# Performance work log

Hardware: AMD Instinct MI355X
Metric: run time of the kernel (lower is better)

The kernel has to match this reference:

```python
import jax, jax.numpy as jnp
import numpy as np

C = 256
HEADS = 4
HIDDEN = 4 * C  # LeFF default hidden_dim = dim*4
EPS = 1e-5


def conv2d(x, w, pad):
    # x: [B,C,H,W], w: [O,I,kh,kw]
    return jax.lax.conv_general_dilated(
        x, w, window_strides=(1, 1), padding=[(pad, pad), (pad, pad)],
        dimension_numbers=('NCHW', 'OIHW', 'NCHW'))


def dwconv2d(x, w, pad):
    # depthwise: w: [C,1,kh,kw], groups = C
    return jax.lax.conv_general_dilated(
        x, w, window_strides=(1, 1), padding=[(pad, pad), (pad, pad)],
        dimension_numbers=('NCHW', 'OIHW', 'NCHW'),
        feature_group_count=x.shape[1])


def conv1x1(x, w):
    # w: [O, I]; pointwise conv as einsum
    return jnp.einsum('oi,bihw->bohw', w, x)


def layernorm(x, weight, bias):
    # WithBias LayerNorm over channel dim of NCHW (matches to_3d -> LN over c)
    mu = jnp.mean(x, axis=1, keepdims=True)
    var = jnp.mean((x - mu) ** 2, axis=1, keepdims=True)
    xn = (x - mu) / jnp.sqrt(var + EPS)
    return xn * weight[None, :, None, None] + bias[None, :, None, None]


def mhsa(q, k, v, heads):
    # q,k,v: [B,C,H,W] -> global attention over N = H*W tokens
    b, c, h, w = q.shape
    d = c // heads
    scale = d ** -0.5
    def split(t):
        return t.reshape(b, heads, d, h * w)  # [B,H,d,N]
    qh, kh, vh = split(q), split(k), split(v)
    attn = jnp.einsum('bhdn,bhdm->bhnm', qh, kh) * scale  # [B,H,N,N]
    attn = jax.nn.softmax(attn, axis=-1)
    out = jnp.einsum('bhnm,bhdm->bhdn', attn, vh)
    return out.reshape(b, c, h, w)


def self_attn(x, w_qkv, w_proj, heads):
    qkv = conv1x1(x, w_qkv)  # [B,3C,H,W]
    q, k, v = jnp.split(qkv, 3, axis=1)
    return conv1x1(mhsa(q, k, v, heads), w_proj)


def cross_attn(qf, kvf, w_q, w_k, w_v, w_proj, heads):
    q = conv1x1(qf, w_q)
    k = conv1x1(kvf, w_k)
    v = conv1x1(kvf, w_v)
    return conv1x1(mhsa(q, k, v, heads), w_proj)


def leff(x, w_in, w_dw, w_out):
    h = conv1x1(x, w_in)
    h = dwconv2d(h, w_dw, pad=1)
    h = jax.nn.gelu(h, approximate=False)  # torch nn.GELU() = exact erf
    return conv1x1(h, w_out)


def setup_inputs() -> dict:
    key = jax.random.key(0)
    ks = jax.random.split(key, 32)
    s = 0.02
    inp = {
        'aop_feat': jax.random.normal(ks[0], (8, C, 32, 32), jnp.float32),
        'dop_feat': jax.random.normal(ks[1], (8, C, 32, 32), jnp.float32),
        'w_qconv': jax.random.normal(ks[2], (C, C, 3, 3), jnp.float32) * s,
        'w_kvconv': jax.random.normal(ks[3], (C, C, 5, 5), jnp.float32) * s,
        'lnq1_w': jnp.ones((C,), jnp.float32), 'lnq1_b': jnp.zeros((C,), jnp.float32),
        'lnkv1_w': jnp.ones((C,), jnp.float32), 'lnkv1_b': jnp.zeros((C,), jnp.float32),
        'lnq2_w': jnp.ones((C,), jnp.float32), 'lnq2_b': jnp.zeros((C,), jnp.float32),
        'lnkv2_w': jnp.ones((C,), jnp.float32), 'lnkv2_b': jnp.zeros((C,), jnp.float32),
        'lnffn_w': jnp.ones((C,), jnp.float32), 'lnffn_b': jnp.zeros((C,), jnp.float32),
        'saq_qkv': jax.random.normal(ks[4], (3 * C, C), jnp.float32) * s,
        'saq_proj': jax.random.normal(ks[5], (C, C), jnp.float32) * s,
        'sakv_qkv': jax.random.normal(ks[6], (3 * C, C), jnp.float32) * s,
        'sakv_proj': jax.random.normal(ks[7], (C, C), jnp.float32) * s,
        'ca_q': jax.random.normal(ks[8], (C, C), jnp.float32) * s,
        'ca_k': jax.random.normal(ks[9], (C, C), jnp.float32) * s,
        'ca_v': jax.random.normal(ks[10], (C, C), jnp.float32) * s,
        'ca_proj': jax.random.normal(ks[11], (C, C), jnp.float32) * s,
        'leff_in': jax.random.normal(ks[12], (HIDDEN, C), jnp.float32) * s,
        'leff_dw': jax.random.normal(ks[13], (HIDDEN, 1, 3, 3), jnp.float32) * s,
        'leff_out': jax.random.normal(ks[14], (C, HIDDEN), jnp.float32) * s,
    }
    return inp


def reference(aop_feat, dop_feat, w_qconv, w_kvconv,
              lnq1_w, lnq1_b, lnkv1_w, lnkv1_b, lnq2_w, lnq2_b,
              lnkv2_w, lnkv2_b, lnffn_w, lnffn_b,
              saq_qkv, saq_proj, sakv_qkv, sakv_proj,
              ca_q, ca_k, ca_v, ca_proj,
              leff_in, leff_dw, leff_out):
    # q branch
    q_branch = conv2d(aop_feat, w_qconv, pad=1)
    q_branch = q_branch + self_attn(layernorm(q_branch, lnq1_w, lnq1_b), saq_qkv, saq_proj, HEADS)
    q = layernorm(q_branch, lnq2_w, lnq2_b)
    # kv branch
    kv_branch = conv2d(dop_feat, w_kvconv, pad=2)
    kv_branch = kv_branch + self_attn(layernorm(kv_branch, lnkv1_w, lnkv1_b), sakv_qkv, sakv_proj, HEADS)
    kv = layernorm(kv_branch, lnkv2_w, lnkv2_b)
    # cross attention + FFN
    x = q_branch + cross_attn(q, kv, ca_q, ca_k, ca_v, ca_proj, HEADS)
    x = x + leff(layernorm(x, lnffn_w, lnffn_b), leff_in, leff_dw, leff_out)
    return x
```

## Files before the change

### kernel.cpp

```cpp
#include <hip/hip_runtime.h>
#include <hip/hip_bf16.h>


using bf16 = __hip_bfloat16;
typedef short v8s __attribute__((ext_vector_type(8)));
typedef float v4f  __attribute__((ext_vector_type(4)));

static __device__ __forceinline__ float bf2f(bf16 x) { return __bfloat162float(x); }
static __device__ __forceinline__ float us2f(unsigned short u)
{ union { unsigned int i; float f; } x; x.i = ((unsigned)u) << 16; return x.f; }
static __device__ __forceinline__ unsigned short f2us(float f)
{ bf16 h = __float2bfloat16(f); return *(unsigned short*)&h; }
static __device__ __forceinline__ float ldi(const void* p, size_t i, int isbf)
{ return isbf ? bf2f(((const bf16*)p)[i]) : ((const float*)p)[i]; }

__global__ void detect_kernel(const unsigned short* p, int* flag)
{
    if (threadIdx.x == 0 && blockIdx.x == 0)
        *flag = (p[0] == 0x3F80) ? 1 : 0;
}

struct CvtArgs { const void* src[20]; unsigned off[21]; };

__global__ __launch_bounds__(256) void cvt_lin(CvtArgs a, const int* __restrict__ flag,
                                               bf16* __restrict__ dst)
{
    unsigned e = blockIdx.x * 256u + threadIdx.x;
    int isbf = *flag;
    int s = 0;
    while (e >= a.off[s + 1]) ++s;
    dst[e] = __float2bfloat16(ldi(a.src[s], e - a.off[s], isbf));
}

__global__ __launch_bounds__(256) void tcvt2(const void* __restrict__ s0,
                                             const void* __restrict__ s1,
                                             const int* __restrict__ flag,
                                             bf16* __restrict__ d0,
                                             bf16* __restrict__ d1)
{
    __shared__ float T[64][65];
    const void* src = (blockIdx.z < 8) ? s0 : s1;
    bf16* dst       = (blockIdx.z < 8) ? d0 : d1;
    int hw0 = blockIdx.x * 64, c0 = blockIdx.y * 64, b = blockIdx.z & 7;
    int t = threadIdx.x, isbf = *flag;
    int c = t >> 2, x16 = (t & 3) * 16;
    size_t sbase = ((size_t)b * 256 + c0 + c) * 1024 + hw0 + x16;
#pragma unroll
    for (int j = 0; j < 16; ++j) T[c][x16 + j] = ldi(src, sbase + j, isbf);
    __syncthreads();
    int hw = t >> 2, c16 = (t & 3) * 16;
    bf16* dp = dst + ((size_t)(b << 10) + hw0 + hw) * 256 + c0 + c16;
#pragma unroll
    for (int j = 0; j < 16; ++j) dp[j] = __float2bfloat16(T[c16 + j][hw]);
}

__global__ __launch_bounds__(256) void repack_all(
    const void* __restrict__ W3, const void* __restrict__ W5,
    const void* __restrict__ Wdw, const int* __restrict__ flag,
    bf16* __restrict__ R3, bf16* __restrict__ R5, bf16* __restrict__ Rdw)
{
    int idx = blockIdx.x * 256 + threadIdx.x;
    int isbf = *flag;
    if (idx < 589824) {
        int ci = idx & 255, o = (idx >> 8) & 255, khkw = idx >> 16;
        int kh = khkw / 3, kw = khkw % 3;
        R3[idx] = __float2bfloat16(
            ldi(W3, (((size_t)o * 256 + ci) * 3 + kh) * 3 + kw, isbf));
    } else if (idx < 2228224) {
        int j = idx - 589824;
        int ci = j & 255, o = (j >> 8) & 255, khkw = j >> 16;
        int kh = khkw / 5, kw = khkw % 5;
        R5[j] = __float2bfloat16(
            ldi(W5, (((size_t)o * 256 + ci) * 5 + kh) * 5 + kw, isbf));
    } else {
        int j = idx - 2228224;
        int c = j & 1023, tap = j >> 10;
        Rdw[j] = __float2bfloat16(ldi(Wdw, (size_t)c * 9 + tap, isbf));
    }
}

static __device__ __forceinline__ void mgemm_core(
    const short* __restrict__ MA, const short* __restrict__ MB,
    bf16* __restrict__ Yb, float* __restrict__ Yf, bf16* __restrict__ Y2,
    const bf16* __restrict__ R, int K, int mode, int Ochan,
    short As[64][72], short Bs[64][72])
{
    int m0 = blockIdx.x * 64, n0 = blockIdx.y * 64;
    int t = threadIdx.x, lane = t & 63, wv = t >> 6;
    int l15 = lane & 15, quad = lane >> 4;
    int srow = t >> 2, scol = (t & 3) * 16;

    const short* pa = &MA[(size_t)(m0 + srow) * K + scol];
    const short* pb = &MB[(size_t)(n0 + srow) * K + scol];

    v4f acc[4] = {};
    v8s ra0 = *(const v8s*)&pa[0], ra1 = *(const v8s*)&pa[8];
    v8s rb0 = *(const v8s*)&pb[0], rb1 = *(const v8s*)&pb[8];

    for (int k0 = 0; k0 < K; k0 += 64) {
        if (k0) __syncthreads();
        *(v8s*)&As[srow][scol]     = ra0;
        *(v8s*)&As[srow][scol + 8] = ra1;
        *(v8s*)&Bs[srow][scol]     = rb0;
        *(v8s*)&Bs[srow][scol + 8] = rb1;
        __syncthreads();
        if (k0 + 64 < K) {
            ra0 = *(const v8s*)&pa[k0 + 64];
            ra1 = *(const v8s*)&pa[k0 + 72];
            rb0 = *(const v8s*)&pb[k0 + 64];
            rb1 = *(const v8s*)&pb[k0 + 72];
        }
#pragma unroll
        for (int kk = 0; kk < 2; ++kk) {
            v8s a = *(const v8s*)&As[wv * 16 + l15][kk * 32 + quad * 8];
#pragma unroll
            for (int nt = 0; nt < 4; ++nt) {
                v8s b = *(const v8s*)&Bs[nt * 16 + l15][kk * 32 + quad * 8];
                acc[nt] = __builtin_amdgcn_mfma_f32_16x16x32_bf16(a, b, acc[nt], 0, 0, 0);
            }
        }
    }

#pragma unroll
    for (int nt = 0; nt < 4; ++nt)
#pragma unroll
        for (int r = 0; r < 4; ++r) {
            int mm = m0 + wv * 16 + quad * 4 + r;
            int nn = n0 + nt * 16 + l15;
            float v = acc[nt][r];
            if (mode == 0) {
                size_t off = (size_t)mm * Ochan + nn;
                if (R) v += bf2f(R[off]);
                Yb[off] = __float2bfloat16(v);
            } else if (mode == 1) {
                Yb[((size_t)(nn >> 10) * Ochan + mm) * 1024 + (nn & 1023)] =
                    __float2bfloat16(v);
            } else if (mode == 2) {
                Yf[((size_t)(nn >> 10) * Ochan + mm) * 1024 + (nn & 1023)] =
                    v + bf2f(R[(size_t)nn * 256 + mm]);
            } else if (mode == 3) {
                if (mm < 512) Yb[(size_t)nn * 512 + mm] = __float2bfloat16(v);
                else Y2[((size_t)(nn >> 10) * 256 + (mm - 512)) * 1024 + (nn & 1023)] =
                         __float2bfloat16(v);
            } else {
                Yb[(size_t)nn * 512 + Ochan + mm] = __float2bfloat16(v);
            }
        }
}

__global__ __launch_bounds__(256) void mgemm(
    const short* __restrict__ MA, const short* __restrict__ MB,
    bf16* __restrict__ Yb, float* __restrict__ Yf, bf16* __restrict__ Y2,
    const bf16* __restrict__ R, int K, int mode, int Ochan)
{
    __shared__ short As[64][72], Bs[64][72];
    mgemm_core(MA, MB, Yb, Yf, Y2, R, K, mode, Ochan, As, Bs);
}

struct GA { const short* A; const short* B; bf16* Yb; float* Yf; bf16* Y2;
            const bf16* R; int K; int mode; int Oc; };
struct GA3 { GA g[3]; };

__global__ __launch_bounds__(256) void mgemm_z(GA3 P)
{
    __shared__ short As[64][72], Bs[64][72];
    const GA& a = P.g[blockIdx.z];
    mgemm_core(a.A, a.B, a.Yb, a.Yf, a.Y2, a.R, a.K, a.mode, a.Oc, As, Bs);
}

template <int KS, int PAD>
static __device__ __forceinline__ void mconv128_core(
    const short* __restrict__ Xn, const short* __restrict__ Wr,
    bf16* __restrict__ Y, float* __restrict__ Yf,
    short As[128][72], short Bs[128][72],
    int p0, int o0, int kbeg, int kend)
{
    int t = threadIdx.x, lane = t & 63, wv = t >> 6;
    int l15 = lane & 15, quad = lane >> 4;
    int wm = wv >> 1, wn = wv & 1;
    int srow = t >> 1, scol = (t & 1) * 32;

    int p  = p0 + srow;
    int hw = p & 1023, hh = hw >> 5, ww = hw & 31;
    size_t ib = ((size_t)(p >> 10)) << 10;

    v4f acc[4][4] = {};
    v8s ra[4], rb[4];

    auto ldk = [&](int k0) {
        int khkw = k0 >> 8;
        int kh = khkw / KS, kw = khkw % KS;
        int hi = hh + kh - PAD, wi = ww + kw - PAD;
        int aci = (k0 & 255) + scol;
        v8s z = {0, 0, 0, 0, 0, 0, 0, 0};
        ra[0] = z; ra[1] = z; ra[2] = z; ra[3] = z;
        if ((unsigned)hi < 32u && (unsigned)wi < 32u) {
            const short* sa = &Xn[(ib + (hi << 5) + wi) * 256 + aci];
            ra[0] = *(const v8s*)&sa[0];  ra[1] = *(const v8s*)&sa[8];
            ra[2] = *(const v8s*)&sa[16]; ra[3] = *(const v8s*)&sa[24];
        }
        const short* sb = &Wr[((size_t)khkw * 256 + o0 + srow) * 256 + (k0 & 255) + scol];
        rb[0] = *(const v8s*)&sb[0];  rb[1] = *(const v8s*)&sb[8];
        rb[2] = *(const v8s*)&sb[16]; rb[3] = *(const v8s*)&sb[24];
    };

    ldk(kbeg);

    for (int k0 = kbeg; k0 < kend; k0 += 64) {
        if (k0 != kbeg) __syncthreads();
        *(v8s*)&As[srow][scol]      = ra[0];
        *(v8s*)&As[srow][scol + 8]  = ra[1];
        *(v8s*)&As[srow][scol + 16] = ra[2];
        *(v8s*)&As[srow][scol + 24] = ra[3];
        *(v8s*)&Bs[srow][scol]      = rb[0];
        *(v8s*)&Bs[srow][scol + 8]  = rb[1];
        *(v8s*)&Bs[srow][scol + 16] = rb[2];
        *(v8s*)&Bs[srow][scol + 24] = rb[3];
        __syncthreads();
        if (k0 + 64 < kend) ldk(k0 + 64);
#pragma unroll
        for (int kk = 0; kk < 2; ++kk) {
            v8s af[4], bf[4];
#pragma unroll
            for (int i = 0; i < 4; ++i)
                af[i] = *(const v8s*)&As[wm * 64 + i * 16 + l15][kk * 32 + quad * 8];
#pragma unroll
            for (int i = 0; i < 4; ++i)
                bf[i] = *(const v8s*)&Bs[wn * 64 + i * 16 + l15][kk * 32 + quad * 8];
#pragma unroll
            for (int mt = 0; mt < 4; ++mt)
#pragma unroll
                for (int nt = 0; nt < 4; ++nt)
                    acc[mt][nt] = __builtin_amdgcn_mfma_f32_16x16x32_bf16(
                        af[mt], bf[nt], acc[mt][nt], 0, 0, 0);
        }
    }

#pragma unroll
    for (int mt = 0; mt < 4; ++mt)
#pragma unroll
        for (int nt = 0; nt < 4; ++nt)
#pragma unroll
            for (int r = 0; r < 4; ++r) {
                int pp = p0 + wm * 64 + mt * 16 + quad * 4 + r;
                int oo = o0 + wn * 64 + nt * 16 + l15;
                if (Yf) Yf[(size_t)pp * 256 + oo] = acc[mt][nt][r];
                else    Y[(size_t)pp * 256 + oo] = __float2bfloat16(acc[mt][nt][r]);
            }
}

__global__ __launch_bounds__(256) void mconv2(
    const short* __restrict__ Xa, const short* __restrict__ Wa, bf16* __restrict__ Ya,
    const short* __restrict__ Xb, const short* __restrict__ Wb,
    float* __restrict__ P0, float* __restrict__ P1, float* __restrict__ P2)
{
    __shared__ short As[128][72];
    __shared__ short Bs[128][72];
    int wg = blockIdx.x;
    if (wg < 128) {
        mconv128_core<3, 1>(Xa, Wa, Ya, nullptr, As, Bs,
                            (wg & 63) * 128, (wg >> 6) * 128, 0, 2304);
    } else {
        int j = wg - 128;
        int part = j >> 7, xy = j & 127;
        float* Pf = (part == 0) ? P0 : (part == 1) ? P1 : P2;
        int kbeg = part * 2112;
        int kend = (part < 2) ? kbeg + 2112 : 6400;
        mconv128_core<5, 2>(Xb, Wb, nullptr, Pf, As, Bs,
                            (xy & 63) * 128, (xy >> 6) * 128, kbeg, kend);
    }
}

__global__ __launch_bounds__(256) void addcvt3(
    const float* __restrict__ A, const float* __restrict__ B,
    const float* __restrict__ C, bf16* __restrict__ Y)
{
    int i = (blockIdx.x * 256 + threadIdx.x) * 4;
    float4 a = *(const float4*)&A[i];
    float4 b = *(const float4*)&B[i];
    float4 c = *(const float4*)&C[i];
    ushort4 o;
    o.x = f2us(a.x + b.x + c.x);
    o.y = f2us(a.y + b.y + c.y);
    o.z = f2us(a.z + b.z + c.z);
    o.w = f2us(a.w + b.w + c.w);
    *(ushort4*)((unsigned short*)Y + i) = o;
}

static __device__ __forceinline__ void attn_core(
    const bf16* __restrict__ QK, const bf16* __restrict__ V,
    bf16* __restrict__ Out, int b, int h, int n0,
    short Ps[4][16][72], short Ks[64][72], short Vs[64][72])
{
    int t = threadIdx.x, lane = t & 63, wv = t >> 6;
    int l15 = lane & 15, quad = lane >> 4;
    int srow = t >> 2, scol = (t & 3) * 16;

    const short* qk = (const short*)QK;
    const short* vp = (const short*)V + ((size_t)b * 256 + h * 64) * 1024;

    size_t qrow = ((size_t)b * 1024 + n0 + wv * 16 + l15) * 512 + h * 64;
    v8s qf0 = *(const v8s*)&qk[qrow + quad * 8];
    v8s qf1 = *(const v8s*)&qk[qrow + 32 + quad * 8];

    v4f oacc[4] = {};
    float mi[4], li[4], nmiSC[4];
#pragma unroll
    for (int r = 0; r < 4; ++r) { mi[r] = -1e30f; li[r] = 0.f; nmiSC[r] = 0.f; }
    const float SC = 0.18033688011112042f;

    const short* kbase = &qk[((size_t)b * 1024 + srow) * 512 + 256 + h * 64 + scol];
    const short* vbase = vp + (size_t)srow * 1024 + scol;

    v8s rk0 = *(const v8s*)&kbase[0], rk1 = *(const v8s*)&kbase[8];
    v8s rv0 = *(const v8s*)&vbase[0], rv1 = *(const v8s*)&vbase[8];

    for (int m0 = 0; m0 < 1024; m0 += 64) {
        if (m0) __syncthreads();
        *(v8s*)&Ks[srow][scol]     = rk0;
        *(v8s*)&Ks[srow][scol + 8] = rk1;
        *(v8s*)&Vs[srow][scol]     = rv0;
        *(v8s*)&Vs[srow][scol + 8] = rv1;
        __syncthreads();
        if (m0 + 64 < 1024) {
            rk0 = *(const v8s*)&kbase[(size_t)(m0 + 64) * 512];
            rk1 = *(const v8s*)&kbase[(size_t)(m0 + 64) * 512 + 8];
            rv0 = *(const v8s*)&vbase[m0 + 64];
            rv1 = *(const v8s*)&vbase[m0 + 72];
        }

        v4f sacc[4];
        __builtin_amdgcn_s_setprio(1);
#pragma unroll
        for (int ct = 0; ct < 4; ++ct) {
            v8s kf0 = *(const v8s*)&Ks[ct * 16 + l15][quad * 8];
            v8s kf1 = *(const v8s*)&Ks[ct * 16 + l15][32 + quad * 8];
            v4f z = {0.f, 0.f, 0.f, 0.f};
            z = __builtin_amdgcn_mfma_f32_16x16x32_bf16(qf0, kf0, z, 0, 0, 0);
            z = __builtin_amdgcn_mfma_f32_16x16x32_bf16(qf1, kf1, z, 0, 0, 0);
            sacc[ct] = z;
        }
        __builtin_amdgcn_s_setprio(0);

        float pr[4];
#pragma unroll
        for (int r = 0; r < 4; ++r)
            pr[r] = fmaxf(fmaxf(sacc[0][r], sacc[1][r]),
                          fmaxf(sacc[2][r], sacc[3][r]));
        bool grow = (pr[0] > mi[0]) | (pr[1] > mi[1]) |
                    (pr[2] > mi[2]) | (pr[3] > mi[3]);
        if (__any(grow)) {
#pragma unroll
            for (int mk = 1; mk <= 8; mk <<= 1)
#pragma unroll
                for (int r = 0; r < 4; ++r)
                    pr[r] = fmaxf(pr[r], __shfl_xor(pr[r], mk));
#pragma unroll
            for (int r = 0; r < 4; ++r) {
                float mn = fmaxf(mi[r], pr[r]);
                float al = exp2f((mi[r] - mn) * SC);
                mi[r] = mn;
                nmiSC[r] = -mn * SC;
                li[r] *= al;
#pragma unroll
                for (int dt = 0; dt < 4; ++dt) oacc[dt][r] *= al;
            }
        }

#pragma unroll
        for (int ct = 0; ct < 4; ++ct)
#pragma unroll
            for (int r = 0; r < 4; ++r) {
                float pvv = exp2f(fmaf(sacc[ct][r], SC, nmiSC[r]));
                li[r] += pvv;
                Ps[wv][quad * 4 + r][ct * 16 + l15] = (short)f2us(pvv);
            }

        v8s pf0 = *(const v8s*)&Ps[wv][l15][quad * 8];
        v8s pf1 = *(const v8s*)&Ps[wv][l15][32 + quad * 8];
        __builtin_amdgcn_s_setprio(1);
#pragma unroll
        for (int dt = 0; dt < 4; ++dt) {
            v8s vf0 = *(const v8s*)&Vs[dt * 16 + l15][quad * 8];
            v8s vf1 = *(const v8s*)&Vs[dt * 16 + l15][32 + quad * 8];
            oacc[dt] = __builtin_amdgcn_mfma_f32_16x16x32_bf16(pf0, vf0, oacc[dt], 0, 0, 0);
            oacc[dt] = __builtin_amdgcn_mfma_f32_16x16x32_bf16(pf1, vf1, oacc[dt], 0, 0, 0);
        }
        __builtin_amdgcn_s_setprio(0);
    }

#pragma unroll
    for (int mk = 1; mk <= 8; mk <<= 1)
#pragma unroll
        for (int r = 0; r < 4; ++r)
            li[r] += __shfl_xor(li[r], mk);

    float linv[4];
#pragma unroll
    for (int r = 0; r < 4; ++r) linv[r] = 1.0f / li[r];
    size_t pb = (size_t)b * 1024 + n0 + wv * 16;
#pragma unroll
    for (int dt = 0; dt < 4; ++dt)
#pragma unroll
        for (int r = 0; r < 4; ++r)
            Out[(pb + quad * 4 + r) * 256 + h * 64 + dt * 16 + l15] =
                __float2bfloat16(oacc[dt][r] * linv[r]);
}

template <int NG>
__global__ __launch_bounds__(256) void attn_swz(
    const bf16* __restrict__ QK0, const bf16* __restrict__ V0, bf16* __restrict__ O0,
    const bf16* __restrict__ QK1, const bf16* __restrict__ V1, bf16* __restrict__ O1)
{
    __shared__ short Ps[4][16][72];
    __shared__ short Ks[64][72], Vs[64][72];
    int i = blockIdx.x;
    int xcd = i & 7, idx = i >> 3;
    int g = xcd * (NG / 8) + (idx >> 4);
    int n0 = (idx & 15) * 64;
    int h = g & 3, zz = g >> 2;
    int b = zz & 7;
    if (zz < 8) attn_core(QK0, V0, O0, b, h, n0, Ps, Ks, Vs);
    else        attn_core(QK1, V1, O1, b, h, n0, Ps, Ks, Vs);
}

static __device__ __forceinline__ void ln_row(
    const bf16* __restrict__ X, const bf16* __restrict__ g,
    const bf16* __restrict__ be, bf16* __restrict__ Y, size_t p)
{
    int lane = threadIdx.x & 63;
    const ushort4 u = *(const ushort4*)(X + p * 256 + lane * 4);
    float v0 = us2f(u.x), v1 = us2f(u.y), v2 = us2f(u.z), v3 = us2f(u.w);
    float s = v0 + v1 + v2 + v3;
    float ss = v0 * v0 + v1 * v1 + v2 * v2 + v3 * v3;
#pragma unroll
    for (int off = 32; off; off >>= 1) {
        s  += __shfl_xor(s, off);
        ss += __shfl_xor(ss, off);
    }
    float mu   = s * (1.0f / 256.0f);
    float var  = ss * (1.0f / 256.0f) - mu * mu;
    float rstd = rsqrtf(fmaxf(var, 0.0f) + 1e-5f);
    const ushort4 gu = *(const ushort4*)((const unsigned short*)g + lane * 4);
    const ushort4 bu = *(const ushort4*)((const unsigned short*)be + lane * 4);
    ushort4 o;
    o.x = f2us((v0 - mu) * rstd * us2f(gu.x) + us2f(bu.x));
    o.y = f2us((v1 - mu) * rstd * us2f(gu.y) + us2f(bu.y));
    o.z = f2us((v2 - mu) * rstd * us2f(gu.z) + us2f(bu.z));
    o.w = f2us((v3 - mu) * rstd * us2f(gu.w) + us2f(bu.w));
    *(ushort4*)(Y + p * 256 + lane * 4) = o;
}

__global__ __launch_bounds__(256) void ln_nhwc(
    const bf16* __restrict__ X, const bf16* __restrict__ g,
    const bf16* __restrict__ be, bf16* __restrict__ Y)
{
    int wv = threadIdx.x >> 6;
    ln_row(X, g, be, Y, (size_t)blockIdx.x * 4 + wv);
}

__global__ __launch_bounds__(256) void ln_nhwc2(
    const bf16* __restrict__ X0, const bf16* __restrict__ g0,
    const bf16* __restrict__ b0, bf16* __restrict__ Y0,
    const bf16* __restrict__ X1, const bf16* __restrict__ g1,
    const bf16* __restrict__ b1, bf16* __restrict__ Y1)
{
    int wv = threadIdx.x >> 6;
    int sel = blockIdx.x >> 11;
    size_t p = (size_t)(blockIdx.x & 2047) * 4 + wv;
    if (sel == 0) ln_row(X0, g0, b0, Y0, p);
    else          ln_row(X1, g1, b1, Y1, p);
}

__global__ __launch_bounds__(256) void dwgelu_nhwc(
    const bf16* __restrict__ H, const bf16* __restrict__ Wr,
    bf16* __restrict__ Y)
{
    int idx = blockIdx.x * 256 + threadIdx.x;
    int p = idx >> 7, c8 = (idx & 127) * 8;
    int hw = p & 1023, hh = hw >> 5, ww = hw & 31;
    size_t ib = ((size_t)(p >> 10)) << 10;
    float acc[8] = {};
#pragma unroll
    for (int kh = 0; kh < 3; ++kh)
#pragma unroll
        for (int kw = 0; kw < 3; ++kw) {
            int hi = hh + kh - 1, wi = ww + kw - 1;
            if ((unsigned)hi < 32u && (unsigned)wi < 32u) {
                v8s hv = *(const v8s*)((const short*)H + (ib + (hi << 5) + wi) * 1024 + c8);
                v8s wvv = *(const v8s*)((const short*)Wr + (kh * 3 + kw) * 1024 + c8);
#pragma unroll
                for (int j = 0; j < 8; ++j)
                    acc[j] = fmaf(us2f((unsigned short)wvv[j]),
                                  us2f((unsigned short)hv[j]), acc[j]);
            }
        }
    short ov[8];
#pragma unroll
    for (int j = 0; j < 8; ++j) {
        float x = acc[j];
        ov[j] = (short)f2us(0.5f * x * (1.0f + erff(x * 0.70710678118654752f)));
    }
    v8s o = {ov[0], ov[1], ov[2], ov[3], ov[4], ov[5], ov[6], ov[7]};
    *(v8s*)((short*)Y + (size_t)p * 1024 + c8) = o;
}

extern "C" void kernel_launch(void* const* d_in, const int* in_sizes, int n_in,
                              void* d_out, int out_size, void* d_ws, size_t ws_size,
                              hipStream_t stream)
{
    static const int  lidx[20] = {4,5,6,7,8,9,10,11,12,13,14,15,16,17,18,19,20,21,22,24};
    static const unsigned lsz[20] = {256,256,256,256,256,256,256,256,256,256,
                                     196608,65536,196608,65536,
                                     65536,65536,65536,65536,262144,262144};
    CvtArgs args;
    unsigned pre[21]; pre[0] = 0;
    for (int i = 0; i < 20; ++i) {
        args.src[i] = d_in[lidx[i]];
        pre[i + 1] = pre[i] + lsz[i];
    }
    for (int i = 0; i < 21; ++i) args.off[i] = pre[i];
    const unsigned ltot = pre[20];

    int*  flag  = (int*)d_ws;
    bf16* canon = (bf16*)d_ws + 128;
    bf16* cn[25];
    for (int i = 0; i < 20; ++i) cn[lidx[i]] = canon + pre[i];

    bf16* Wr3  = canon + ltot;
    bf16* Wr5  = Wr3 + 589824;
    bf16* Wdwr = Wr5 + 1638400;
    const size_t SZ = 2097152;
    bf16* slab = Wdwr + 9216;
    bf16* qb   = slab + 0 * SZ;
    bf16* kvb  = slab + 1 * SZ;
    bf16* t0   = slab + 2 * SZ;
    bf16* q    = slab + 3 * SZ;
    bf16* kv   = slab + 4 * SZ;
    bf16* QKb  = slab + 5 * SZ;
    bf16* Vb   = slab + 7 * SZ;
    bf16* t1   = slab + 8 * SZ;
    bf16* QK2  = slab + 9 * SZ;
    bf16* V2   = slab + 11 * SZ;
    bf16* aopT = slab + 9 * SZ;
    bf16* dopT = slab + 10 * SZ;
    bf16* hb   = slab + 3 * SZ;
    bf16* h2   = slab + 7 * SZ;
    float* P0f = (float*)(slab + 2 * SZ);
    float* P1f = (float*)(slab + 4 * SZ);
    float* P2f = (float*)(slab + 6 * SZ);
    float* out = (float*)d_out;

    dim3 blk(256);
    auto S = [](const bf16* p) { return (const short*)p; };

    detect_kernel<<<1, 64, 0, stream>>>((const unsigned short*)d_in[4], flag);
    cvt_lin<<<ltot / 256, blk, 0, stream>>>(args, flag, canon);
    tcvt2<<<dim3(16, 4, 16), blk, 0, stream>>>(d_in[0], d_in[1], flag, aopT, dopT);
    repack_all<<<8740, blk, 0, stream>>>(d_in[2], d_in[3], d_in[23], flag, Wr3, Wr5, Wdwr);

    mconv2<<<512, blk, 0, stream>>>(S(aopT), (const short*)Wr3, qb,
                                    S(dopT), (const short*)Wr5, P0f, P1f, P2f);
    addcvt3<<<2048, blk, 0, stream>>>(P0f, P1f, P2f, kvb);

    ln_nhwc2<<<4096, blk, 0, stream>>>(qb, cn[4], cn[5], t0,
                                       kvb, cn[6], cn[7], t1);
    GA3 P;
    P.g[0] = GA{S(cn[14]), S(t0), QKb, nullptr, Vb, nullptr, 256, 3, 0};
    P.g[1] = GA{S(cn[16]), S(t1), QK2, nullptr, V2, nullptr, 256, 3, 0};
    P.g[2] = P.g[1];
    mgemm_z<<<dim3(12, 128, 2), blk, 0, stream>>>(P);

    attn_swz<64><<<1024, blk, 0, stream>>>(QKb, Vb, t0, QK2, V2, t1);

    P.g[0] = GA{S(t0), S(cn[15]), qb, nullptr, nullptr, qb, 256, 0, 256};
    P.g[1] = GA{S(t1), S(cn[17]), kvb, nullptr, nullptr, kvb, 256, 0, 256};
    P.g[2] = P.g[1];
    mgemm_z<<<dim3(128, 4, 2), blk, 0, stream>>>(P);

    ln_nhwc2<<<4096, blk, 0, stream>>>(qb, cn[8], cn[9], q,
                                       kvb, cn[10], cn[11], kv);

    P.g[0] = GA{S(cn[18]), S(q),  QKb, nullptr, nullptr, nullptr, 256, 4, 0};
    P.g[1] = GA{S(cn[19]), S(kv), QKb, nullptr, nullptr, nullptr, 256, 4, 256};
    P.g[2] = GA{S(cn[20]), S(kv), Vb,  nullptr, nullptr, nullptr, 256, 1, 256};
    mgemm_z<<<dim3(4, 128, 3), blk, 0, stream>>>(P);

    attn_swz<32><<<512, blk, 0, stream>>>(QKb, Vb, t0, QKb, Vb, t0);
    mgemm<<<dim3(128, 4), blk, 0, stream>>>(S(t0), S(cn[21]), qb, nullptr, nullptr, qb, 256, 0, 256);

    ln_nhwc<<<2048, blk, 0, stream>>>(qb, cn[12], cn[13], t0);
    mgemm<<<dim3(128, 16), blk, 0, stream>>>(S(t0), S(cn[22]), hb, nullptr, nullptr, nullptr, 256, 0, 1024);
    dwgelu_nhwc<<<4096, blk, 0, stream>>>(hb, Wdwr, h2);
    mgemm<<<dim3(4, 128), blk, 0, stream>>>(S(cn[24]), S(h2), nullptr, out, nullptr, qb, 1024, 2, 256);
}
```

Measured before the change: 408.6 us.

## Merge preprocessing kernels and add 128x128-tile GEMM for QKV and FFN-in

```diff
diff --git a/kernel.cpp b/kernel.cpp
--- a/kernel.cpp
+++ b/kernel.cpp
@@ -22,60 +22,80 @@
 
 struct CvtArgs { const void* src[20]; unsigned off[21]; };
 
-__global__ __launch_bounds__(256) void cvt_lin(CvtArgs a, const int* __restrict__ flag,
-                                               bf16* __restrict__ dst)
-{
-    unsigned e = blockIdx.x * 256u + threadIdx.x;
-    int isbf = *flag;
-    int s = 0;
-    while (e >= a.off[s + 1]) ++s;
-    dst[e] = __float2bfloat16(ldi(a.src[s], e - a.off[s], isbf));
-}
-
-__global__ __launch_bounds__(256) void tcvt2(const void* __restrict__ s0,
-                                             const void* __restrict__ s1,
-                                             const int* __restrict__ flag,
-                                             bf16* __restrict__ d0,
-                                             bf16* __restrict__ d1)
-{
-    __shared__ float T[64][65];
-    const void* src = (blockIdx.z < 8) ? s0 : s1;
-    bf16* dst       = (blockIdx.z < 8) ? d0 : d1;
-    int hw0 = blockIdx.x * 64, c0 = blockIdx.y * 64, b = blockIdx.z & 7;
-    int t = threadIdx.x, isbf = *flag;
-    int c = t >> 2, x16 = (t & 3) * 16;
-    size_t sbase = ((size_t)b * 256 + c0 + c) * 1024 + hw0 + x16;
-#pragma unroll
-    for (int j = 0; j < 16; ++j) T[c][x16 + j] = ldi(src, sbase + j, isbf);
-    __syncthreads();
-    int hw = t >> 2, c16 = (t & 3) * 16;
-    bf16* dp = dst + ((size_t)(b << 10) + hw0 + hw) * 256 + c0 + c16;
-#pragma unroll
-    for (int j = 0; j < 16; ++j) dp[j] = __float2bfloat16(T[c16 + j][hw]);
-}
-
-__global__ __launch_bounds__(256) void repack_all(
+__global__ __launch_bounds__(256) void pre_all(
+    CvtArgs a,
+    const void* __restrict__ s0, const void* __restrict__ s1,
     const void* __restrict__ W3, const void* __restrict__ W5,
     const void* __restrict__ Wdw, const int* __restrict__ flag,
+    bf16* __restrict__ canon,
+    bf16* __restrict__ d0, bf16* __restrict__ d1,
     bf16* __restrict__ R3, bf16* __restrict__ R5, bf16* __restrict__ Rdw)
 {
-    int idx = blockIdx.x * 256 + threadIdx.x;
+    __shared__ float T[64][65];
+    int bx = blockIdx.x, t = threadIdx.x;
     int isbf = *flag;
-    if (idx < 589824) {
-        int ci = idx & 255, o = (idx >> 8) & 255, khkw = idx >> 16;
-        int kh = khkw / 3, kw = khkw % 3;
-        R3[idx] = __float2bfloat16(
-            ldi(W3, (((size_t)o * 256 + ci) * 3 + kh) * 3 + kw, isbf));
-    } else if (idx < 2228224) {
-        int j = idx - 589824;
-        int ci = j & 255, o = (j >> 8) & 255, khkw = j >> 16;
-        int kh = khkw / 5, kw = khkw % 5;
-        R5[j] = __float2bfloat16(
-            ldi(W5, (((size_t)o * 256 + ci) * 5 + kh) * 5 + kw, isbf));
+    if (bx < 5130) {
+        unsigned e = bx * 256u + t;
+        int s = 0;
+        while (e >= a.off[s + 1]) ++s;
+        canon[e] = __float2bfloat16(ldi(a.src[s], e - a.off[s], isbf));
+    } else if (bx < 6154) {
+        int i = bx - 5130;
+        int x = i & 15, y = (i >> 4) & 3, z = i >> 6;
+        const void* src = (z < 8) ? s0 : s1;
+        bf16* dst       = (z < 8) ? d0 : d1;
+        int hw0 = x * 64, c0 = y * 64, b = z & 7;
+        int c = t >> 2, x16 = (t & 3) * 16;
+        size_t sbase = ((size_t)b * 256 + c0 + c) * 1024 + hw0 + x16;
+#pragma unroll
+        for (int j = 0; j < 16; ++j) T[c][x16 + j] = ldi(src, sbase + j, isbf);
+        __syncthreads();
+        int hw = t >> 2, c16 = (t & 3) * 16;
+        bf16* dp = dst + ((size_t)(b << 10) + hw0 + hw) * 256 + c0 + c16;
+#pragma unroll
+        for (int j = 0; j < 16; ++j) dp[j] = __float2bfloat16(T[c16 + j][hw]);
     } else {
-        int j = idx - 2228224;
-        int c = j & 1023, tap = j >> 10;
-        Rdw[j] = __float2bfloat16(ldi(Wdw, (size_t)c * 9 + tap, isbf));
+        int idx = (bx - 6154) * 256 + t;
+        if (idx < 589824) {
+            int ci = idx & 255, o = (idx >> 8) & 255, khkw = idx >> 16;
+            int kh = khkw / 3, kw = khkw % 3;
+            R3[idx] = __float2bfloat16(
+                ldi(W3, (((size_t)o * 256 + ci) * 3 + kh) * 3 + kw, isbf));
+        } else if (idx < 2228224) {
+            int j = idx - 589824;
+            int ci = j & 255, o = (j >> 8) & 255, khkw = j >> 16;
+            int kh = khkw / 5, kw = khkw % 5;
+            R5[j] = __float2bfloat16(
+                ldi(W5, (((size_t)o * 256 + ci) * 5 + kh) * 5 + kw, isbf));
+        } else {
+            int j = idx - 2228224;
+            int c = j & 1023, tap = j >> 10;
+            Rdw[j] = __float2bfloat16(ldi(Wdw, (size_t)c * 9 + tap, isbf));
+        }
+    }
+}
+
+static __device__ __forceinline__ void gemm_store(
+    bf16* __restrict__ Yb, float* __restrict__ Yf, bf16* __restrict__ Y2,
+    const bf16* __restrict__ R, int mode, int Ochan,
+    int mm, int nn, float v)
+{
+    if (mode == 0) {
+        size_t off = (size_t)mm * Ochan + nn;
+        if (R) v += bf2f(R[off]);
+        Yb[off] = __float2bfloat16(v);
+    } else if (mode == 1) {
+        Yb[((size_t)(nn >> 10) * Ochan + mm) * 1024 + (nn & 1023)] =
+            __float2bfloat16(v);
+    } else if (mode == 2) {
+        Yf[((size_t)(nn >> 10) * Ochan + mm) * 1024 + (nn & 1023)] =
+            v + bf2f(R[(size_t)nn * 256 + mm]);
+    } else if (mode == 3) {
+        if (mm < 512) Yb[(size_t)nn * 512 + mm] = __float2bfloat16(v);
+        else Y2[((size_t)(nn >> 10) * 256 + (mm - 512)) * 1024 + (nn & 1023)] =
+                 __float2bfloat16(v);
+    } else {
+        Yb[(size_t)nn * 512 + Ochan + mm] = __float2bfloat16(v);
     }
 }
 
@@ -124,28 +144,10 @@
 #pragma unroll
     for (int nt = 0; nt < 4; ++nt)
 #pragma unroll
-        for (int r = 0; r < 4; ++r) {
-            int mm = m0 + wv * 16 + quad * 4 + r;
-            int nn = n0 + nt * 16 + l15;
-            float v = acc[nt][r];
-            if (mode == 0) {
-                size_t off = (size_t)mm * Ochan + nn;
-                if (R) v += bf2f(R[off]);
-                Yb[off] = __float2bfloat16(v);
-            } else if (mode == 1) {
-                Yb[((size_t)(nn >> 10) * Ochan + mm) * 1024 + (nn & 1023)] =
-                    __float2bfloat16(v);
-            } else if (mode == 2) {
-                Yf[((size_t)(nn >> 10) * Ochan + mm) * 1024 + (nn & 1023)] =
-                    v + bf2f(R[(size_t)nn * 256 + mm]);
-            } else if (mode == 3) {
-                if (mm < 512) Yb[(size_t)nn * 512 + mm] = __float2bfloat16(v);
-                else Y2[((size_t)(nn >> 10) * 256 + (mm - 512)) * 1024 + (nn & 1023)] =
-                         __float2bfloat16(v);
-            } else {
-                Yb[(size_t)nn * 512 + Ochan + mm] = __float2bfloat16(v);
-            }
-        }
+        for (int r = 0; r < 4; ++r)
+            gemm_store(Yb, Yf, Y2, R, mode, Ochan,
+                       m0 + wv * 16 + quad * 4 + r,
+                       n0 + nt * 16 + l15, acc[nt][r]);
 }
 
 __global__ __launch_bounds__(256) void mgemm(
@@ -166,6 +168,83 @@
     __shared__ short As[64][72], Bs[64][72];
     const GA& a = P.g[blockIdx.z];
     mgemm_core(a.A, a.B, a.Yb, a.Yf, a.Y2, a.R, a.K, a.mode, a.Oc, As, Bs);
+}
+
+static __device__ __forceinline__ void mgemm128_core(
+    const short* __restrict__ MA, const short* __restrict__ MB,
+    bf16* __restrict__ Yb, float* __restrict__ Yf, bf16* __restrict__ Y2,
+    const bf16* __restrict__ R, int K, int mode, int Ochan,
+    short As[128][72], short Bs[128][72])
+{
+    int m0 = blockIdx.x * 128, n0 = blockIdx.y * 128;
+    int t = threadIdx.x, lane = t & 63, wv = t >> 6;
+    int l15 = lane & 15, quad = lane >> 4;
+    int wm = wv >> 1, wn = wv & 1;
+    int srow = t >> 1, scol = (t & 1) * 32;
+
+    const short* pa = &MA[(size_t)(m0 + srow) * K + scol];
+    const short* pb = &MB[(size_t)(n0 + srow) * K + scol];
+
+    v4f acc[4][4] = {};
+    v8s ra[4], rb[4];
+    ra[0] = *(const v8s*)&pa[0];  ra[1] = *(const v8s*)&pa[8];
+    ra[2] = *(const v8s*)&pa[16]; ra[3] = *(const v8s*)&pa[24];
+    rb[0] = *(const v8s*)&pb[0];  rb[1] = *(const v8s*)&pb[8];
+    rb[2] = *(const v8s*)&pb[16]; rb[3] = *(const v8s*)&pb[24];
+
+    for (int k0 = 0; k0 < K; k0 += 64) {
+        if (k0) __syncthreads();
+        *(v8s*)&As[srow][scol]      = ra[0];
+        *(v8s*)&As[srow][scol + 8]  = ra[1];
+        *(v8s*)&As[srow][scol + 16] = ra[2];
+        *(v8s*)&As[srow][scol + 24] = ra[3];
+        *(v8s*)&Bs[srow][scol]      = rb[0];
+        *(v8s*)&Bs[srow][scol + 8]  = rb[1];
+        *(v8s*)&Bs[srow][scol + 16] = rb[2];
+        *(v8s*)&Bs[srow][scol + 24] = rb[3];
+        __syncthreads();
+        if (k0 + 64 < K) {
+            const short* a2 = pa + k0 + 64;
+            ra[0] = *(const v8s*)&a2[0];  ra[1] = *(const v8s*)&a2[8];
+            ra[2] = *(const v8s*)&a2[16]; ra[3] = *(const v8s*)&a2[24];
+            const short* b2 = pb + k0 + 64;
+            rb[0] = *(const v8s*)&b2[0];  rb[1] = *(const v8s*)&b2[8];
+            rb[2] = *(const v8s*)&b2[16]; rb[3] = *(const v8s*)&b2[24];
+        }
+#pragma unroll
+        for (int kk = 0; kk < 2; ++kk) {
+            v8s af[4], bf[4];
+#pragma unroll
+            for (int i = 0; i < 4; ++i)
+                af[i] = *(const v8s*)&As[wm * 64 + i * 16 + l15][kk * 32 + quad * 8];
+#pragma unroll
+            for (int i = 0; i < 4; ++i)
+                bf[i] = *(const v8s*)&Bs[wn * 64 + i * 16 + l15][kk * 32 + quad * 8];
+#pragma unroll
+            for (int mt = 0; mt < 4; ++mt)
+#pragma unroll
+                for (int nt = 0; nt < 4; ++nt)
+                    acc[mt][nt] = __builtin_amdgcn_mfma_f32_16x16x32_bf16(
+                        af[mt], bf[nt], acc[mt][nt], 0, 0, 0);
+        }
+    }
+
+#pragma unroll
+    for (int mt = 0; mt < 4; ++mt)
+#pragma unroll
+        for (int nt = 0; nt < 4; ++nt)
+#pragma unroll
+            for (int r = 0; r < 4; ++r)
+                gemm_store(Yb, Yf, Y2, R, mode, Ochan,
+                           m0 + wm * 64 + mt * 16 + quad * 4 + r,
+                           n0 + wn * 64 + nt * 16 + l15, acc[mt][nt][r]);
+}
+
+__global__ __launch_bounds__(256) void mgemm128_z(GA3 P)
+{
+    __shared__ short As[128][72], Bs[128][72];
+    const GA& a = P.g[blockIdx.z];
+    mgemm128_core(a.A, a.B, a.Yb, a.Yf, a.Y2, a.R, a.K, a.mode, a.Oc, As, Bs);
 }
 
 template <int KS, int PAD>
@@ -555,9 +634,9 @@
     auto S = [](const bf16* p) { return (const short*)p; };
 
     detect_kernel<<<1, 64, 0, stream>>>((const unsigned short*)d_in[4], flag);
-    cvt_lin<<<ltot / 256, blk, 0, stream>>>(args, flag, canon);
-    tcvt2<<<dim3(16, 4, 16), blk, 0, stream>>>(d_in[0], d_in[1], flag, aopT, dopT);
-    repack_all<<<8740, blk, 0, stream>>>(d_in[2], d_in[3], d_in[23], flag, Wr3, Wr5, Wdwr);
+    pre_all<<<5130 + 1024 + 8740, blk, 0, stream>>>(
+        args, d_in[0], d_in[1], d_in[2], d_in[3], d_in[23], flag,
+        canon, aopT, dopT, Wr3, Wr5, Wdwr);
 
     mconv2<<<512, blk, 0, stream>>>(S(aopT), (const short*)Wr3, qb,
                                     S(dopT), (const short*)Wr5, P0f, P1f, P2f);
@@ -569,7 +648,7 @@
     P.g[0] = GA{S(cn[14]), S(t0), QKb, nullptr, Vb, nullptr, 256, 3, 0};
     P.g[1] = GA{S(cn[16]), S(t1), QK2, nullptr, V2, nullptr, 256, 3, 0};
     P.g[2] = P.g[1];
-    mgemm_z<<<dim3(12, 128, 2), blk, 0, stream>>>(P);
+    mgemm128_z<<<dim3(6, 64, 2), blk, 0, stream>>>(P);
 
     attn_swz<64><<<1024, blk, 0, stream>>>(QKb, Vb, t0, QK2, V2, t1);
 
@@ -590,7 +669,10 @@
     mgemm<<<dim3(128, 4), blk, 0, stream>>>(S(t0), S(cn[21]), qb, nullptr, nullptr, qb, 256, 0, 256);
 
     ln_nhwc<<<2048, blk, 0, stream>>>(qb, cn[12], cn[13], t0);
-    mgemm<<<dim3(128, 16), blk, 0, stream>>>(S(t0), S(cn[22]), hb, nullptr, nullptr, nullptr, 256, 0, 1024);
+    P.g[0] = GA{S(t0), S(cn[22]), hb, nullptr, nullptr, nullptr, 256, 0, 1024};
+    P.g[1] = P.g[0];
+    P.g[2] = P.g[0];
+    mgemm128_z<<<dim3(64, 8, 1), blk, 0, stream>>>(P);
     dwgelu_nhwc<<<4096, blk, 0, stream>>>(hb, Wdwr, h2);
     mgemm<<<dim3(4, 128), blk, 0, stream>>>(S(cn[24]), S(h2), nullptr, out, nullptr, qb, 1024, 2, 256);
 }
```

Result: slower. 420.0 us (+2.8%).
